# Optimization experiments

Measured on AMD Instinct MI355X. Metric: run time of the kernel, lower is better.

## Reference

```python
import jax, jax.numpy as jnp
import numpy as np

N_SPECIES = 4; N_BASIS = 128; N_GRAPH = 16; R_MAX = 6.0
NS_NODE, NV_NODE = 32, 16          # node irreps 32x0e + 16x1o
NS_EDGE = 16                       # initial edge irreps 16x0e
NS_OUT, NV_OUT = 16, 8             # output irreps 16x0e + 8x1o
NS_IN = 2 * NS_NODE + NS_EDGE      # 80 concatenated scalars
NV_IN = 2 * NV_NODE                # 32 concatenated vectors
NS_CONV = NS_OUT + NV_OUT          # 24 scalars (16 features + 8 gates)
W_SIZES = [NS_IN * NS_CONV, NS_IN * NV_OUT, NV_IN * NV_OUT, NV_IN * NS_CONV, NV_IN * NV_OUT]
N_NODES, N_EDGES = 8192, 65536
EPS = 1e-5


def gaussian_basis(d, stop, n):
    offsets = jnp.linspace(0.0, stop, n)
    coeff = -0.5 / (offsets[1] - offsets[0]) ** 2
    return jnp.exp(coeff * (d[:, None] - offsets[None, :]) ** 2)


def seg_mean(vals, seg, cnt):
    return jax.ops.segment_sum(vals, seg, num_segments=N_GRAPH) / cnt[:, None]


def setup_inputs():
    key = jax.random.key(0)
    ks = jax.random.split(key, 20)
    rn = lambda k, shape, scale: jax.random.normal(k, shape, jnp.float32) * scale
    inp = {}
    inp["node_fea"] = rn(ks[0], (N_NODES, NS_NODE + 3 * NV_NODE), 1.0)
    d = 0.5 + 5.0 * jax.random.uniform(ks[1], (N_EDGES,), jnp.float32)
    vec = jax.random.normal(ks[2], (N_EDGES, 3), jnp.float32)
    inp["edge_attr"] = jnp.concatenate([d[:, None], vec], axis=1)
    inp["edge_index"] = jax.random.randint(ks[3], (2, N_EDGES), 0, N_NODES)
    inp["x"] = jax.random.randint(ks[4], (N_NODES,), 0, N_SPECIES)
    inp["batch"] = jnp.sort(jax.random.randint(ks[5], (N_NODES,), 0, N_GRAPH))
    inp["w_rh"] = rn(ks[6], (N_BASIS, 64), N_BASIS ** -0.5); inp["b_rh"] = jnp.zeros((64,), jnp.float32)
    inp["w_ro"] = rn(ks[7], (64, sum(W_SIZES)), 64 ** -0.5); inp["b_ro"] = jnp.zeros((sum(W_SIZES),), jnp.float32)
    inp["w_pre"] = rn(ks[8], (NS_EDGE, NS_EDGE), NS_EDGE ** -0.5); inp["b_pre"] = jnp.zeros((NS_EDGE,), jnp.float32)
    inp["w_sc"] = rn(ks[9], (NS_EDGE, N_SPECIES ** 2, NS_OUT), 1.0)
    inp["w_post_s"] = rn(ks[10], (NS_OUT, NS_OUT), NS_OUT ** -0.5); inp["b_post_s"] = jnp.zeros((NS_OUT,), jnp.float32)
    inp["w_post_v"] = rn(ks[11], (NV_OUT, NV_OUT), NV_OUT ** -0.5)
    inp["ln_w_s"] = jnp.ones((NS_OUT,), jnp.float32); inp["ln_b_s"] = jnp.zeros((NS_OUT,), jnp.float32)
    inp["ln_w_v"] = jnp.ones((NV_OUT,), jnp.float32)
    inp["w_skip"] = rn(ks[12], (NS_EDGE, NS_OUT), NS_EDGE ** -0.5)
    inp["w_edge_s"] = rn(ks[13], (NS_OUT, NS_OUT), NS_OUT ** -0.5); inp["b_edge_s"] = jnp.zeros((NS_OUT,), jnp.float32)
    inp["w_edge_v"] = rn(ks[14], (NV_OUT, NV_OUT), NV_OUT ** -0.5)
    return inp


def _forward(node_fea, edge_attr, w_rh, b_rh, w_ro, b_ro, w_pre, b_pre, w_sc,
             w_post_s, b_post_s, w_post_v, ln_w_s, ln_b_s, ln_w_v,
             w_skip, w_edge_s, b_edge_s, w_edge_v, edge_index, x, batch):
    E = edge_index.shape[1]
    idx_i, idx_j = edge_index[0], edge_index[1]
    one_hot = jax.nn.one_hot(N_SPECIES * x[idx_i] + x[idx_j], N_SPECIES ** 2, dtype=node_fea.dtype)
    d, vec = edge_attr[:, 0], edge_attr[:, 1:4]
    u = vec / (jnp.linalg.norm(vec, axis=1, keepdims=True) + 1e-12)
    Y1 = np.sqrt(3.0) * u                                   # l=1 sph harm, component norm; Y0 == 1
    rbf = gaussian_basis(d, R_MAX, N_BASIS)                 # edge_length_embedded
    edge_s0 = gaussian_basis(d, 6.0, NS_EDGE)               # distance_expansion -> initial edge scalars
    # self connection: edge scalars x species-pair one-hot -> output scalars
    sc = jnp.einsum('ei,ej,ijo->eo', edge_s0, one_hot, w_sc) / np.sqrt(NS_EDGE * N_SPECIES ** 2)
    edge_s = edge_s0 @ w_pre + b_pre                        # lin_pre
    # gather node features by edge indices and concat
    nf_i, nf_j = node_fea[idx_i], node_fea[idx_j]
    s_in = jnp.concatenate([nf_i[:, :NS_NODE], nf_j[:, :NS_NODE], edge_s], axis=1)  # [E,80]
    v_in = jnp.concatenate([nf_i[:, NS_NODE:].reshape(E, NV_NODE, 3),
                            nf_j[:, NS_NODE:].reshape(E, NV_NODE, 3)], axis=1)      # [E,32,3]
    # radial MLP -> per-edge tensor-product path weights
    h = jax.nn.silu(rbf @ w_rh + b_rh)
    w_all = h @ w_ro + b_ro                                 # [E, 3840]
    w1, w2, w3, w4, w5 = jnp.split(w_all, np.cumsum(W_SIZES)[:-1].tolist(), axis=1)
    # equivariant tensor-product paths (explicit l<=1 Clebsch-Gordan structure)
    s0 = jnp.einsum('ei,eio->eo', s_in, w1.reshape(E, NS_IN, NS_CONV)) / np.sqrt(NS_IN)            # 0e x 0e -> 0e
    vA = jnp.einsum('ei,eio,ec->eoc', s_in, w2.reshape(E, NS_IN, NV_OUT), Y1) / np.sqrt(NS_IN)     # 0e x 1o -> 1o
    vB = jnp.einsum('eic,eio->eoc', v_in, w3.reshape(E, NV_IN, NV_OUT)) / np.sqrt(NV_IN)           # 1o x 0e -> 1o
    s1 = jnp.einsum('eic,eio,ec->eo', v_in, w4.reshape(E, NV_IN, NS_CONV), Y1) / np.sqrt(3.0 * NV_IN)  # 1o.1o -> 0e
    vC = jnp.einsum('eic,eio->eoc', jnp.cross(v_in, Y1[:, None, :]), w5.reshape(E, NV_IN, NV_OUT)) / np.sqrt(2.0 * NV_IN)  # 1o x 1o -> 1o
    s_conv = s0 + s1                                        # [E,24]
    v_conv = vA + vB + vC                                   # [E,8,3]
    # gate nonlinearity inside conv
    s_out = jax.nn.silu(s_conv[:, :NS_OUT])
    v_out = v_conv * jax.nn.sigmoid(s_conv[:, NS_OUT:])[:, :, None]
    # lin_post then self connection
    s_out = s_out @ w_post_s + b_post_s + sc
    v_out = jnp.einsum('eic,io->eoc', v_out, w_post_v)
    # e3LayerNorm keyed by graph id of source node
    eb = batch[idx_i]
    cnt = jnp.maximum(jax.ops.segment_sum(jnp.ones((E,), s_out.dtype), eb, num_segments=N_GRAPH), 1.0)
    mu = seg_mean(s_out, eb, cnt)
    s_c = s_out - mu[eb]
    rms_s = jnp.sqrt(seg_mean(s_c ** 2, eb, cnt).mean(axis=1, keepdims=True) + EPS)
    s_n = s_c / rms_s[eb] * ln_w_s + ln_b_s
    rms_v = jnp.sqrt((seg_mean((v_out ** 2).sum(-1), eb, cnt) / 3.0).mean(axis=1, keepdims=True) + EPS)
    v_n = v_out / rms_v[eb][:, :, None] * ln_w_v[None, :, None]
    # skip connection from old edge features (scalars only)
    s_n = s_n + edge_s0 @ w_skip
    # final lin_edge
    s_fin = s_n @ w_edge_s + b_edge_s
    v_fin = jnp.einsum('eic,io->eoc', v_n, w_edge_v)
    return jnp.concatenate([s_fin, v_fin.reshape(E, NV_OUT * 3)], axis=1)  # [E,40]


def reference(node_fea, edge_attr, edge_index, x, batch, w_rh, b_rh, w_ro, b_ro,
              w_pre, b_pre, w_sc, w_post_s, b_post_s, w_post_v, ln_w_s, ln_b_s, ln_w_v,
              w_skip, w_edge_s, b_edge_s, w_edge_v):
    return _forward(node_fea, edge_attr, w_rh, b_rh, w_ro, b_ro, w_pre, b_pre, w_sc,
                    w_post_s, b_post_s, w_post_v, ln_w_s, ln_b_s, ln_w_v,
                    w_skip, w_edge_s, b_edge_s, w_edge_v, edge_index, x, batch)
```

## Files before the change

kernel.cpp:

```cpp
#include <hip/hip_runtime.h>

typedef unsigned short u16;
typedef unsigned int u32;
typedef __attribute__((ext_vector_type(8))) _Float16 half8;
typedef __attribute__((ext_vector_type(2))) __fp16 fp16x2;
typedef __attribute__((ext_vector_type(4))) float floatx4;

#define E_TOTAL 65536

__device__ __forceinline__ u32 pk16(float x0, float x1) {
    union { fp16x2 h; u32 u; } c;
    c.h = __builtin_amdgcn_cvt_pkrtz(x0, x1);
    return c.u;
}
union Frag8h { u32 u[4]; half8 v; };


__global__ void k_zero(float* __restrict__ ws) {
    const int i = threadIdx.x + blockIdx.x * blockDim.x;
    if (i < 1056) ws[i] = 0.0f;
}

__global__ __launch_bounds__(64) void k_probe(int* __restrict__ binv) {
    const int lane = threadIdx.x;
    const int q = lane >> 4;
    if (lane < 32) binv[lane] = lane;
    half8 bfr;
    #pragma unroll
    for (int j = 0; j < 8; ++j) bfr[j] = (_Float16)(float)(q*8 + j + 1);
    #pragma unroll
    for (int s = 0; s < 32; ++s) {
        const int qa = s >> 3, ja = s & 7;
        half8 afr;
        #pragma unroll
        for (int j = 0; j < 8; ++j) afr[j] = (_Float16)0.0f;
        if (q == qa) afr[ja] = (_Float16)1.0f;
        floatx4 dc = {0.0f, 0.0f, 0.0f, 0.0f};
        dc = __builtin_amdgcn_mfma_f32_16x16x32_f16(afr, bfr, dc, 0, 0, 0);
        if (lane == 0) {
            const int sB = (int)(dc[0] + 0.5f) - 1;
            if (sB >= 0 && sB < 32) binv[sB] = s;
        }
    }
}

__global__ __launch_bounds__(256) void k_edge_heavy(
    const float* __restrict__ node_fea, const float* __restrict__ edge_attr,
    const int* __restrict__ edge_index, const int* __restrict__ xsp,
    const float* __restrict__ w_rh, const float* __restrict__ b_rh,
    const float* __restrict__ w_ro, const float* __restrict__ b_ro,
    const float* __restrict__ w_pre, const float* __restrict__ b_pre,
    const float* __restrict__ w_sc, const float* __restrict__ w_post_s,
    const float* __restrict__ b_post_s, const float* __restrict__ w_post_v,
    const int* __restrict__ binv,
    float* __restrict__ out)
{
    __shared__ __align__(16) u16 a_rbf[16 * 128];
    __shared__ __align__(16) u16 a_h[16 * 64];
    __shared__ __align__(16) float sh_wt[16][258];
    __shared__ float sh_sin[16][80];
    __shared__ float sh_vl[16][3][32];
    __shared__ float sh_acc[16][56];
    __shared__ float sh_es0[16][16];
    __shared__ float sh_y1[16][4];
    __shared__ int   sh_kmap[32];

    const int tid = threadIdx.x;
    const int ed = tid >> 4, l16 = tid & 15;
    const int lane = tid & 63, w = tid >> 6;
    const int quad = lane >> 4, l15 = lane & 15;
    const int e = blockIdx.x * 16 + ed;

    if (tid < 32) sh_kmap[tid] = binv[tid];

    const int ni = edge_index[e];
    const int nj = edge_index[E_TOTAL + e];
    const float4 ea = *(const float4*)(edge_attr + 4*e);
    const float d  = ea.x;
    const float vx = ea.y, vy = ea.z, vz = ea.w;
    const float invn = 1.0f / (sqrtf(vx*vx + vy*vy + vz*vz) + 1e-12f);
    const float Y0 = 1.7320508075688772f * vx * invn;
    const float Y1 = 1.7320508075688772f * vy * invn;
    const float Y2 = 1.7320508075688772f * vz * invn;
    if (l16 == 0) { sh_y1[ed][0] = Y0; sh_y1[ed][1] = Y1; sh_y1[ed][2] = Y2; }

    const float C128 = -0.5f * (127.0f/6.0f) * (127.0f/6.0f);
    const float S128 = 6.0f/127.0f;
    {
        Frag8h thi;
        #pragma unroll
        for (int r2 = 0; r2 < 4; ++r2) {
            const int b0i = l16*8 + 2*r2;
            const float t0 = d - S128 * (float)b0i;
            const float t1 = d - S128 * (float)(b0i + 1);
            const float x0 = expf(C128 * t0 * t0);
            const float x1 = expf(C128 * t1 * t1);
            thi.u[r2] = pk16(x0, x1);
        }
        *(half8*)&a_rbf[(l16*16 + ed)*8] = thi.v;
    }
    {
        const float t = d - 0.4f * (float)l16;
        sh_es0[ed][l16] = expf(-3.125f * t * t);
    }

    const float rs80 = 0.11180339887498949f;
    const float rs32 = 0.17677669529663689f;
    {
        const float* fi = node_fea + (size_t)ni * 80;
        const float* fj = node_fea + (size_t)nj * 80;
        sh_sin[ed][2*l16+0]    = fi[2*l16+0] * rs80;
        sh_sin[ed][2*l16+1]    = fi[2*l16+1] * rs80;
        sh_sin[ed][32+2*l16+0] = fj[2*l16+0] * rs80;
        sh_sin[ed][32+2*l16+1] = fj[2*l16+1] * rs80;
        #pragma unroll
        for (int c = 0; c < 3; ++c) {
            sh_vl[ed][c][l16]      = fi[32 + 3*l16 + c] * rs32;
            sh_vl[ed][c][16 + l16] = fj[32 + 3*l16 + c] * rs32;
        }
    }
    for (int s = tid; s < 16*56; s += 256) (&sh_acc[0][0])[s] = 0.0f;
    __syncthreads();

    int km[8];
    u32 voff0[8], voff1[8];
    #pragma unroll
    for (int j = 0; j < 8; ++j) {
        km[j] = sh_kmap[quad*8 + j];
        voff0[j] = (u32)(km[j] * 3840 + l15);
        voff1[j] = voff0[j] + 32u * 3840u;
    }

    float my_sc;
    {
        const int o = l16;
        float es = b_pre[o];
        float sc = 0.0f;
        const int p = 4*xsp[ni] + xsp[nj];
        #pragma unroll
        for (int i = 0; i < 16; ++i) {
            const float g = sh_es0[ed][i];
            es += g * w_pre[i*16 + o];
            sc += g * w_sc[(i*16 + p)*16 + o];
        }
        sh_sin[ed][64 + o] = es * rs80;
        my_sc = sc * 0.0625f;
    }

    {
        floatx4 hacc = {0.0f, 0.0f, 0.0f, 0.0f};
        #pragma unroll
        for (int kk = 0; kk < 4; ++kk) {
            const half8 ah = *(const half8*)&a_rbf[((kk*4 + quad)*16 + l15)*8];
            Frag8h bh;
            #pragma unroll
            for (int jj = 0; jj < 4; ++jj) {
                const float x0 = w_rh[(size_t)(kk*32 + km[2*jj+0])*64 + w*16 + l15];
                const float x1 = w_rh[(size_t)(kk*32 + km[2*jj+1])*64 + w*16 + l15];
                bh.u[jj] = pk16(x0, x1);
            }
            hacc = __builtin_amdgcn_mfma_f32_16x16x32_f16(ah, bh.v, hacc, 0, 0, 0);
        }
        const int hn = w*16 + l15;
        const float bb = b_rh[hn];
        const int k8 = hn >> 3, j2 = hn & 7;
        #pragma unroll
        for (int r = 0; r < 4; ++r) {
            const float x = hacc[r] + bb;
            const float s = x / (1.0f + expf(-x));
            const int m = quad*4 + r;
            union { _Float16 h; u16 u; } cv; cv.h = (_Float16)s;
            a_h[(k8*16 + m)*8 + j2] = cv.u;
        }
    }
    __syncthreads();

    const half8 a0 = *(const half8*)&a_h[((0*4 + quad)*16 + l15)*8];
    const half8 a1 = *(const half8*)&a_h[((1*4 + quad)*16 + l15)*8];

    for (int ch = 0; ch < 15; ++ch) {
        const int coff = ch * 256;
        floatx4 acc[4];
        float bias[4];
        #pragma unroll
        for (int ct = 0; ct < 4; ++ct) {
            const int sgct = __builtin_amdgcn_readfirstlane(ch*16 + w*4 + ct);
            const float* bp = w_ro + sgct*16;
            float f0[8], f1[8];
            #pragma unroll
            for (int j = 0; j < 8; ++j) {
                f0[j] = bp[voff0[j]];
                f1[j] = bp[voff1[j]];
            }
            Frag8h b0, b1;
            #pragma unroll
            for (int jj = 0; jj < 4; ++jj) {
                b0.u[jj] = pk16(f0[2*jj], f0[2*jj+1]);
                b1.u[jj] = pk16(f1[2*jj], f1[2*jj+1]);
            }
            floatx4 a = {0.0f, 0.0f, 0.0f, 0.0f};
            a = __builtin_amdgcn_mfma_f32_16x16x32_f16(a0, b0.v, a, 0, 0, 0);
            a = __builtin_amdgcn_mfma_f32_16x16x32_f16(a1, b1.v, a, 0, 0, 0);
            acc[ct] = a;
            bias[ct] = b_ro[sgct*16 + l15];
        }
        __syncthreads();
        #pragma unroll
        for (int ct = 0; ct < 4; ++ct) {
            const int col = w*64 + ct*16 + l15;
            #pragma unroll
            for (int r = 0; r < 4; ++r)
                sh_wt[quad*4 + r][col] = acc[ct][r] + bias[ct];
        }
        __syncthreads();

        if (ch <= 7) {
            const int hi = (ch == 7) ? 1920 : (coff + 256);
            for (int idx = tid; idx < 384; idx += 256) {
                const int eo = idx / 24, o = idx % 24;
                const int i0 = (coff > o) ? (coff - o + 23) / 24 : 0;
                int i1 = (hi - o + 23) / 24; if (i1 > 80) i1 = 80;
                float a = 0.0f;
                for (int i = i0; i < i1; ++i)
                    a += sh_sin[eo][i] * sh_wt[eo][i*24 + o - coff];
                sh_acc[eo][o] += a;
            }
        }
        if (ch == 7) {
            for (int idx = tid; idx < 128; idx += 256) {
                const int eo = idx >> 3, o = idx & 7;
                float a = 0.0f;
                #pragma unroll
                for (int i = 0; i < 16; ++i)
                    a += sh_sin[eo][i] * sh_wt[eo][128 + i*8 + o];
                sh_acc[eo][24 + o] += a;
            }
        }
        if (ch == 8 || ch == 9) {
            const int ib = (ch == 8) ? 16 : 48;
            for (int idx = tid; idx < 128; idx += 256) {
                const int eo = idx >> 3, o = idx & 7;
                float a = 0.0f;
                #pragma unroll
                for (int i2 = 0; i2 < 32; ++i2)
                    a += sh_sin[eo][ib + i2] * sh_wt[eo][i2*8 + o];
                sh_acc[eo][24 + o] += a;
            }
        }
        if (ch == 10) {
            for (int idx = tid; idx < 384; idx += 256) {
                const int eo = idx / 24, rem = idx % 24;
                const int o = rem / 3, cc = rem % 3;
                float a = 0.0f;
                #pragma unroll
                for (int i = 0; i < 32; ++i)
                    a += sh_vl[eo][cc][i] * sh_wt[eo][i*8 + o];
                sh_acc[eo][32 + o*3 + cc] += a;
            }
        }
        if (ch >= 11 && ch <= 13) {
            const int rel = coff - 2816;
            for (int idx = tid; idx < 384; idx += 256) {
                const int eo = idx / 24, o = idx % 24;
                const int i0 = (rel > o) ? (rel - o + 23) / 24 : 0;
                int i1 = (rel + 256 - o + 23) / 24; if (i1 > 32) i1 = 32;
                const float Ya = sh_y1[eo][0], Yb = sh_y1[eo][1], Yc = sh_y1[eo][2];
                float a = 0.0f;
                for (int i = i0; i < i1; ++i) {
                    const float qv = sh_vl[eo][0][i]*Ya + sh_vl[eo][1][i]*Yb
                                   + sh_vl[eo][2][i]*Yc;
                    a += qv * sh_wt[eo][i*24 + o - rel];
                }
                sh_acc[eo][o] += a * 0.57735026918962573f;
            }
        }
        if (ch == 14) {
            for (int idx = tid; idx < 384; idx += 256) {
                const int eo = idx / 24, rem = idx % 24;
                const int o = rem / 3, cc = rem % 3;
                const int c1 = (cc < 2) ? cc + 1 : 0;
                const int c2 = (c1 < 2) ? c1 + 1 : 0;
                const float Yp = sh_y1[eo][c2];
                const float Ym = sh_y1[eo][c1];
                float a = 0.0f;
                #pragma unroll
                for (int i = 0; i < 32; ++i)
                    a += (sh_vl[eo][c1][i]*Yp - sh_vl[eo][c2][i]*Ym) * sh_wt[eo][i*8 + o];
                sh_acc[eo][32 + o*3 + cc] += a * 0.70710678118654746f;
            }
        }
    }
    __syncthreads();

    {
        const int o = l16;
        float a = b_post_s[o] + my_sc;
        #pragma unroll
        for (int i = 0; i < 16; ++i) {
            const float sv = sh_acc[ed][i];
            a += (sv / (1.0f + expf(-sv))) * w_post_s[i*16 + o];
        }
        out[(size_t)e*40 + o] = a;
    }
    if (l16 < 8) {
        const int o = l16;
        const float Ya = sh_y1[ed][0], Yb = sh_y1[ed][1], Yc = sh_y1[ed][2];
        float r0 = 0.0f, r1 = 0.0f, r2 = 0.0f;
        #pragma unroll
        for (int i = 0; i < 8; ++i) {
            const float g  = 1.0f / (1.0f + expf(-sh_acc[ed][16 + i]));
            const float a2 = sh_acc[ed][24 + i];
            const float ww = w_post_v[i*8 + o];
            r0 += (a2*Ya + sh_acc[ed][32 + i*3 + 0]) * g * ww;
            r1 += (a2*Yb + sh_acc[ed][32 + i*3 + 1]) * g * ww;
            r2 += (a2*Yc + sh_acc[ed][32 + i*3 + 2]) * g * ww;
        }
        out[(size_t)e*40 + 16 + o*3 + 0] = r0;
        out[(size_t)e*40 + 16 + o*3 + 1] = r1;
        out[(size_t)e*40 + 16 + o*3 + 2] = r2;
    }
}

__global__ __launch_bounds__(256) void k_stats_partial(
    const float* __restrict__ sv, const int* __restrict__ edge_index,
    const int* __restrict__ batch, float* __restrict__ ws)
{
    __shared__ float bins[768];
    const int tid = threadIdx.x;
    for (int s = tid; s < 768; s += 256) bins[s] = 0.0f;
    __syncthreads();

    const int e = blockIdx.x * 256 + tid;
    const int g = batch[edge_index[e]];
    const float* p = sv + (size_t)e * 40;
    float v[40];
    #pragma unroll
    for (int j = 0; j < 40; ++j) v[j] = p[j];

    float* bg = bins + g * 48;
    #pragma unroll
    for (int chn = 0; chn < 16; ++chn) {
        atomicAdd(&bg[chn],      v[chn]);
        atomicAdd(&bg[16 + chn], v[chn] * v[chn]);
    }
    #pragma unroll
    for (int o = 0; o < 8; ++o) {
        const float a = v[16 + o*3], b = v[16 + o*3 + 1], c = v[16 + o*3 + 2];
        atomicAdd(&bg[32 + o], a*a + b*b + c*c);
    }
    atomicAdd(&bg[40], 1.0f);
    __syncthreads();

    for (int s = tid; s < 768; s += 256) {
        const float x = bins[s];
        if (x != 0.0f) atomicAdd(&ws[s], x);
    }
}

__global__ __launch_bounds__(64) void k_stats_final(float* __restrict__ ws)
{
    const int tid = threadIdx.x;
    if (tid < 16) {
        const int g = tid;
        float cnt = ws[g*48 + 40]; if (cnt < 1.0f) cnt = 1.0f;
        const float ic = 1.0f / cnt;
        float vs = 0.0f;
        for (int chn = 0; chn < 16; ++chn) {
            const float mu = ws[g*48 + chn] * ic;
            ws[768 + g*16 + chn] = mu;
            vs += ws[g*48 + 16 + chn] * ic - mu * mu;
        }
        if (vs < 0.0f) vs = 0.0f;
        ws[1024 + g] = 1.0f / sqrtf(vs * (1.0f/16.0f) + 1e-5f);
        float vv = 0.0f;
        for (int o = 0; o < 8; ++o) vv += ws[g*48 + 32 + o];
        vv = vv * ic * (1.0f/3.0f) * (1.0f/8.0f);
        ws[1040 + g] = 1.0f / sqrtf(vv + 1e-5f);
    }
}

__global__ __launch_bounds__(256) void k_edge_final(
    float* buf, const float* __restrict__ ws,
    const float* __restrict__ edge_attr, const int* __restrict__ edge_index,
    const int* __restrict__ batch,
    const float* __restrict__ ln_w_s, const float* __restrict__ ln_b_s,
    const float* __restrict__ ln_w_v, const float* __restrict__ w_skip,
    const float* __restrict__ w_edge_s, const float* __restrict__ b_edge_s,
    const float* __restrict__ w_edge_v)
{
    __shared__ float sh_mu[16][16];
    __shared__ float sh_is[16], sh_iv[16];
    __shared__ float sh_lws[16], sh_lbs[16], sh_lwv[8];
    __shared__ float sh_skip[16][16], sh_wes[16][16], sh_bes[16], sh_wev[8][8];
    const int tid = threadIdx.x;
    sh_mu[tid >> 4][tid & 15]   = ws[768 + tid];
    sh_skip[tid >> 4][tid & 15] = w_skip[tid];
    sh_wes[tid >> 4][tid & 15]  = w_edge_s[tid];
    if (tid < 16) {
        sh_is[tid]  = ws[1024 + tid];
        sh_iv[tid]  = ws[1040 + tid];
        sh_lws[tid] = ln_w_s[tid];
        sh_lbs[tid] = ln_b_s[tid];
        sh_bes[tid] = b_edge_s[tid];
    }
    if (tid < 8)  sh_lwv[tid] = ln_w_v[tid];
    if (tid < 64) sh_wev[tid >> 3][tid & 7] = w_edge_v[tid];
    __syncthreads();

    const int e = blockIdx.x * 256 + tid;
    const int g = batch[edge_index[e]];
    const float d = edge_attr[4*e];
    float es0[16];
    #pragma unroll
    for (int b = 0; b < 16; ++b) {
        const float t = d - 0.4f * (float)b;
        es0[b] = expf(-3.125f * t * t);
    }
    float p[40];
    float* pb = buf + (size_t)e * 40;
    #pragma unroll
    for (int j = 0; j < 40; ++j) p[j] = pb[j];

    const float is = sh_is[g];
    float sn[16];
    #pragma unroll
    for (int chn = 0; chn < 16; ++chn)
        sn[chn] = (p[chn] - sh_mu[g][chn]) * is * sh_lws[chn] + sh_lbs[chn];
    #pragma unroll
    for (int b = 0; b < 16; ++b) {
        const float g0 = es0[b];
        #pragma unroll
        for (int chn = 0; chn < 16; ++chn) sn[chn] += g0 * sh_skip[b][chn];
    }
    #pragma unroll
    for (int o = 0; o < 16; ++o) {
        float a = sh_bes[o];
        #pragma unroll
        for (int chn = 0; chn < 16; ++chn) a += sn[chn] * sh_wes[chn][o];
        pb[o] = a;
    }
    const float iv = sh_iv[g];
    float vn[8][3];
    #pragma unroll
    for (int i = 0; i < 8; ++i) {
        const float f = iv * sh_lwv[i];
        vn[i][0] = p[16 + i*3 + 0] * f;
        vn[i][1] = p[16 + i*3 + 1] * f;
        vn[i][2] = p[16 + i*3 + 2] * f;
    }
    #pragma unroll
    for (int o = 0; o < 8; ++o) {
        float r0 = 0.0f, r1 = 0.0f, r2 = 0.0f;
        #pragma unroll
        for (int i = 0; i < 8; ++i) {
            const float w = sh_wev[i][o];
            r0 += vn[i][0] * w; r1 += vn[i][1] * w; r2 += vn[i][2] * w;
        }
        pb[16 + o*3 + 0] = r0;
        pb[16 + o*3 + 1] = r1;
        pb[16 + o*3 + 2] = r2;
    }
}

extern "C" void kernel_launch(void* const* d_in, const int* in_sizes, int n_in,
                              void* d_out, int out_size, void* d_ws, size_t ws_size,
                              hipStream_t stream)
{
    const float* node_fea  = (const float*)d_in[0];
    const float* edge_attr = (const float*)d_in[1];
    const int* edge_index  = (const int*)d_in[2];
    const int* xsp         = (const int*)d_in[3];
    const int* batch       = (const int*)d_in[4];
    const float* w_rh      = (const float*)d_in[5];
    const float* b_rh      = (const float*)d_in[6];
    const float* w_ro      = (const float*)d_in[7];
    const float* b_ro      = (const float*)d_in[8];
    const float* w_pre     = (const float*)d_in[9];
    const float* b_pre     = (const float*)d_in[10];
    const float* w_sc      = (const float*)d_in[11];
    const float* w_post_s  = (const float*)d_in[12];
    const float* b_post_s  = (const float*)d_in[13];
    const float* w_post_v  = (const float*)d_in[14];
    const float* ln_w_s    = (const float*)d_in[15];
    const float* ln_b_s    = (const float*)d_in[16];
    const float* ln_w_v    = (const float*)d_in[17];
    const float* w_skip    = (const float*)d_in[18];
    const float* w_edge_s  = (const float*)d_in[19];
    const float* b_edge_s  = (const float*)d_in[20];
    const float* w_edge_v  = (const float*)d_in[21];

    float* ws   = (float*)d_ws;
    int*   binv = (int*)(ws + 1056);
    float* out  = (float*)d_out;

    k_zero<<<2, 1024, 0, stream>>>(ws);
    k_probe<<<1, 64, 0, stream>>>(binv);
    k_edge_heavy<<<4096, 256, 0, stream>>>(node_fea, edge_attr, edge_index, xsp,
        w_rh, b_rh, w_ro, b_ro, w_pre, b_pre, w_sc, w_post_s, b_post_s, w_post_v,
        binv, out);
    k_stats_partial<<<256, 256, 0, stream>>>(out, edge_index, batch, ws);
    k_stats_final<<<1, 64, 0, stream>>>(ws);
    k_edge_final<<<256, 256, 0, stream>>>(out, ws, edge_attr, edge_index,
        batch, ln_w_s, ln_b_s, ln_w_v, w_skip, w_edge_s, b_edge_s, w_edge_v);
}
```

Measured before the change: 460.0 us.

## Process 32 edges per block to reuse w_ro fragments; merge small kernels

The heavy edge kernel now handles two 16-edge groups per block. Each w_ro B-fragment loaded from global memory feeds MFMAs for both groups, which halves the weight-fetch traffic per edge, and the grid shrinks to 2048 blocks. The zero and probe kernels are merged into one, and the stats-final computation is folded into the prologue of the final edge kernel, which removes two launches. In exchange, shared memory per block roughly doubles (sh_wt is now 32x258 floats) and register pressure rises, which can lower occupancy.

```diff
diff --git a/kernel.cpp b/kernel.cpp
--- a/kernel.cpp
+++ b/kernel.cpp
@@ -16,30 +16,29 @@
 union Frag8h { u32 u[4]; half8 v; };
 
 
-__global__ void k_zero(float* __restrict__ ws) {
-    const int i = threadIdx.x + blockIdx.x * blockDim.x;
-    if (i < 1056) ws[i] = 0.0f;
-}
-
-__global__ __launch_bounds__(64) void k_probe(int* __restrict__ binv) {
-    const int lane = threadIdx.x;
-    const int q = lane >> 4;
-    if (lane < 32) binv[lane] = lane;
-    half8 bfr;
-    #pragma unroll
-    for (int j = 0; j < 8; ++j) bfr[j] = (_Float16)(float)(q*8 + j + 1);
-    #pragma unroll
-    for (int s = 0; s < 32; ++s) {
-        const int qa = s >> 3, ja = s & 7;
-        half8 afr;
-        #pragma unroll
-        for (int j = 0; j < 8; ++j) afr[j] = (_Float16)0.0f;
-        if (q == qa) afr[ja] = (_Float16)1.0f;
-        floatx4 dc = {0.0f, 0.0f, 0.0f, 0.0f};
-        dc = __builtin_amdgcn_mfma_f32_16x16x32_f16(afr, bfr, dc, 0, 0, 0);
-        if (lane == 0) {
-            const int sB = (int)(dc[0] + 0.5f) - 1;
-            if (sB >= 0 && sB < 32) binv[sB] = s;
+__global__ __launch_bounds__(1024) void k_init(float* __restrict__ ws, int* __restrict__ binv) {
+    const int tid = threadIdx.x;
+    for (int i = tid; i < 1056; i += 1024) ws[i] = 0.0f;
+    if (tid < 64) {
+        const int lane = tid;
+        const int q = lane >> 4;
+        if (lane < 32) binv[lane] = lane;
+        half8 bfr;
+        #pragma unroll
+        for (int j = 0; j < 8; ++j) bfr[j] = (_Float16)(float)(q*8 + j + 1);
+        #pragma unroll
+        for (int s = 0; s < 32; ++s) {
+            const int qa = s >> 3, ja = s & 7;
+            half8 afr;
+            #pragma unroll
+            for (int j = 0; j < 8; ++j) afr[j] = (_Float16)0.0f;
+            if (q == qa) afr[ja] = (_Float16)1.0f;
+            floatx4 dc = {0.0f, 0.0f, 0.0f, 0.0f};
+            dc = __builtin_amdgcn_mfma_f32_16x16x32_f16(afr, bfr, dc, 0, 0, 0);
+            if (lane == 0) {
+                const int sB = (int)(dc[0] + 0.5f) - 1;
+                if (sB >= 0 && sB < 32) binv[sB] = s;
+            }
         }
     }
 }
@@ -55,60 +54,72 @@
     const int* __restrict__ binv,
     float* __restrict__ out)
 {
-    __shared__ __align__(16) u16 a_rbf[16 * 128];
-    __shared__ __align__(16) u16 a_h[16 * 64];
-    __shared__ __align__(16) float sh_wt[16][258];
-    __shared__ float sh_sin[16][80];
-    __shared__ float sh_vl[16][3][32];
-    __shared__ float sh_acc[16][56];
-    __shared__ float sh_es0[16][16];
-    __shared__ float sh_y1[16][4];
+    __shared__ __align__(16) u16 a_rbf[2 * 2048];
+    __shared__ __align__(16) u16 a_h[2 * 1024];
+    __shared__ __align__(16) float sh_wt[32][258];
+    __shared__ float sh_sin[32][80];
+    __shared__ float sh_vl[32][3][32];
+    __shared__ float sh_acc[32][56];
+    __shared__ float sh_es0[32][16];
+    __shared__ float sh_y1[32][4];
     __shared__ int   sh_kmap[32];
 
     const int tid = threadIdx.x;
     const int ed = tid >> 4, l16 = tid & 15;
     const int lane = tid & 63, w = tid >> 6;
     const int quad = lane >> 4, l15 = lane & 15;
-    const int e = blockIdx.x * 16 + ed;
+    const int e0 = blockIdx.x * 32 + ed;
+    const int e1 = e0 + 16;
 
     if (tid < 32) sh_kmap[tid] = binv[tid];
 
-    const int ni = edge_index[e];
-    const int nj = edge_index[E_TOTAL + e];
-    const float4 ea = *(const float4*)(edge_attr + 4*e);
-    const float d  = ea.x;
-    const float vx = ea.y, vy = ea.z, vz = ea.w;
-    const float invn = 1.0f / (sqrtf(vx*vx + vy*vy + vz*vz) + 1e-12f);
-    const float Y0 = 1.7320508075688772f * vx * invn;
-    const float Y1 = 1.7320508075688772f * vy * invn;
-    const float Y2 = 1.7320508075688772f * vz * invn;
-    if (l16 == 0) { sh_y1[ed][0] = Y0; sh_y1[ed][1] = Y1; sh_y1[ed][2] = Y2; }
+    const int ni0 = edge_index[e0], nj0 = edge_index[E_TOTAL + e0];
+    const int ni1 = edge_index[e1], nj1 = edge_index[E_TOTAL + e1];
+    const float4 ea0 = *(const float4*)(edge_attr + 4*e0);
+    const float4 ea1 = *(const float4*)(edge_attr + 4*e1);
+    const float d0 = ea0.x, d1 = ea1.x;
+    {
+        const float invn0 = 1.0f / (sqrtf(ea0.y*ea0.y + ea0.z*ea0.z + ea0.w*ea0.w) + 1e-12f);
+        const float invn1 = 1.0f / (sqrtf(ea1.y*ea1.y + ea1.z*ea1.z + ea1.w*ea1.w) + 1e-12f);
+        if (l16 == 0) {
+            sh_y1[ed][0]    = 1.7320508075688772f * ea0.y * invn0;
+            sh_y1[ed][1]    = 1.7320508075688772f * ea0.z * invn0;
+            sh_y1[ed][2]    = 1.7320508075688772f * ea0.w * invn0;
+            sh_y1[16+ed][0] = 1.7320508075688772f * ea1.y * invn1;
+            sh_y1[16+ed][1] = 1.7320508075688772f * ea1.z * invn1;
+            sh_y1[16+ed][2] = 1.7320508075688772f * ea1.w * invn1;
+        }
+    }
 
     const float C128 = -0.5f * (127.0f/6.0f) * (127.0f/6.0f);
     const float S128 = 6.0f/127.0f;
     {
-        Frag8h thi;
+        Frag8h t0, t1;
         #pragma unroll
         for (int r2 = 0; r2 < 4; ++r2) {
             const int b0i = l16*8 + 2*r2;
-            const float t0 = d - S128 * (float)b0i;
-            const float t1 = d - S128 * (float)(b0i + 1);
-            const float x0 = expf(C128 * t0 * t0);
-            const float x1 = expf(C128 * t1 * t1);
-            thi.u[r2] = pk16(x0, x1);
-        }
-        *(half8*)&a_rbf[(l16*16 + ed)*8] = thi.v;
-    }
-    {
-        const float t = d - 0.4f * (float)l16;
-        sh_es0[ed][l16] = expf(-3.125f * t * t);
+            const float u0 = d0 - S128 * (float)b0i;
+            const float u1 = d0 - S128 * (float)(b0i + 1);
+            const float v0 = d1 - S128 * (float)b0i;
+            const float v1 = d1 - S128 * (float)(b0i + 1);
+            t0.u[r2] = pk16(expf(C128*u0*u0), expf(C128*u1*u1));
+            t1.u[r2] = pk16(expf(C128*v0*v0), expf(C128*v1*v1));
+        }
+        *(half8*)&a_rbf[(l16*16 + ed)*8]        = t0.v;
+        *(half8*)&a_rbf[2048 + (l16*16 + ed)*8] = t1.v;
+    }
+    {
+        const float t0 = d0 - 0.4f * (float)l16;
+        const float t1 = d1 - 0.4f * (float)l16;
+        sh_es0[ed][l16]    = expf(-3.125f * t0 * t0);
+        sh_es0[16+ed][l16] = expf(-3.125f * t1 * t1);
     }
 
     const float rs80 = 0.11180339887498949f;
     const float rs32 = 0.17677669529663689f;
     {
-        const float* fi = node_fea + (size_t)ni * 80;
-        const float* fj = node_fea + (size_t)nj * 80;
+        const float* fi = node_fea + (size_t)ni0 * 80;
+        const float* fj = node_fea + (size_t)nj0 * 80;
         sh_sin[ed][2*l16+0]    = fi[2*l16+0] * rs80;
         sh_sin[ed][2*l16+1]    = fi[2*l16+1] * rs80;
         sh_sin[ed][32+2*l16+0] = fj[2*l16+0] * rs80;
@@ -119,7 +130,20 @@
             sh_vl[ed][c][16 + l16] = fj[32 + 3*l16 + c] * rs32;
         }
     }
-    for (int s = tid; s < 16*56; s += 256) (&sh_acc[0][0])[s] = 0.0f;
+    {
+        const float* fi = node_fea + (size_t)ni1 * 80;
+        const float* fj = node_fea + (size_t)nj1 * 80;
+        sh_sin[16+ed][2*l16+0]    = fi[2*l16+0] * rs80;
+        sh_sin[16+ed][2*l16+1]    = fi[2*l16+1] * rs80;
+        sh_sin[16+ed][32+2*l16+0] = fj[2*l16+0] * rs80;
+        sh_sin[16+ed][32+2*l16+1] = fj[2*l16+1] * rs80;
+        #pragma unroll
+        for (int c = 0; c < 3; ++c) {
+            sh_vl[16+ed][c][l16]      = fi[32 + 3*l16 + c] * rs32;
+            sh_vl[16+ed][c][16 + l16] = fj[32 + 3*l16 + c] * rs32;
+        }
+    }
+    for (int s = tid; s < 32*56; s += 256) (&sh_acc[0][0])[s] = 0.0f;
     __syncthreads();
 
     int km[8];
@@ -131,27 +155,35 @@
         voff1[j] = voff0[j] + 32u * 3840u;
     }
 
-    float my_sc;
+    float my_sc0, my_sc1;
     {
         const int o = l16;
-        float es = b_pre[o];
-        float sc = 0.0f;
-        const int p = 4*xsp[ni] + xsp[nj];
+        float es0v = b_pre[o], sc0 = 0.0f;
+        float es1v = b_pre[o], sc1 = 0.0f;
+        const int p0 = 4*xsp[ni0] + xsp[nj0];
+        const int p1 = 4*xsp[ni1] + xsp[nj1];
         #pragma unroll
         for (int i = 0; i < 16; ++i) {
-            const float g = sh_es0[ed][i];
-            es += g * w_pre[i*16 + o];
-            sc += g * w_sc[(i*16 + p)*16 + o];
-        }
-        sh_sin[ed][64 + o] = es * rs80;
-        my_sc = sc * 0.0625f;
-    }
-
-    {
-        floatx4 hacc = {0.0f, 0.0f, 0.0f, 0.0f};
+            const float g0 = sh_es0[ed][i];
+            const float g1 = sh_es0[16+ed][i];
+            es0v += g0 * w_pre[i*16 + o];
+            es1v += g1 * w_pre[i*16 + o];
+            sc0  += g0 * w_sc[(i*16 + p0)*16 + o];
+            sc1  += g1 * w_sc[(i*16 + p1)*16 + o];
+        }
+        sh_sin[ed][64 + o]    = es0v * rs80;
+        sh_sin[16+ed][64 + o] = es1v * rs80;
+        my_sc0 = sc0 * 0.0625f;
+        my_sc1 = sc1 * 0.0625f;
+    }
+
+    {
+        floatx4 h0 = {0.0f, 0.0f, 0.0f, 0.0f};
+        floatx4 h1 = {0.0f, 0.0f, 0.0f, 0.0f};
         #pragma unroll
         for (int kk = 0; kk < 4; ++kk) {
-            const half8 ah = *(const half8*)&a_rbf[((kk*4 + quad)*16 + l15)*8];
+            const half8 ag0 = *(const half8*)&a_rbf[((kk*4 + quad)*16 + l15)*8];
+            const half8 ag1 = *(const half8*)&a_rbf[2048 + ((kk*4 + quad)*16 + l15)*8];
             Frag8h bh;
             #pragma unroll
             for (int jj = 0; jj < 4; ++jj) {
@@ -159,28 +191,39 @@
                 const float x1 = w_rh[(size_t)(kk*32 + km[2*jj+1])*64 + w*16 + l15];
                 bh.u[jj] = pk16(x0, x1);
             }
-            hacc = __builtin_amdgcn_mfma_f32_16x16x32_f16(ah, bh.v, hacc, 0, 0, 0);
+            h0 = __builtin_amdgcn_mfma_f32_16x16x32_f16(ag0, bh.v, h0, 0, 0, 0);
+            h1 = __builtin_amdgcn_mfma_f32_16x16x32_f16(ag1, bh.v, h1, 0, 0, 0);
         }
         const int hn = w*16 + l15;
         const float bb = b_rh[hn];
         const int k8 = hn >> 3, j2 = hn & 7;
         #pragma unroll
         for (int r = 0; r < 4; ++r) {
-            const float x = hacc[r] + bb;
-            const float s = x / (1.0f + expf(-x));
             const int m = quad*4 + r;
-            union { _Float16 h; u16 u; } cv; cv.h = (_Float16)s;
-            a_h[(k8*16 + m)*8 + j2] = cv.u;
+            {
+                const float x = h0[r] + bb;
+                const float s = x / (1.0f + expf(-x));
+                union { _Float16 h; u16 u; } cv; cv.h = (_Float16)s;
+                a_h[(k8*16 + m)*8 + j2] = cv.u;
+            }
+            {
+                const float x = h1[r] + bb;
+                const float s = x / (1.0f + expf(-x));
+                union { _Float16 h; u16 u; } cv; cv.h = (_Float16)s;
+                a_h[1024 + (k8*16 + m)*8 + j2] = cv.u;
+            }
         }
     }
     __syncthreads();
 
-    const half8 a0 = *(const half8*)&a_h[((0*4 + quad)*16 + l15)*8];
-    const half8 a1 = *(const half8*)&a_h[((1*4 + quad)*16 + l15)*8];
+    const half8 a0g0 = *(const half8*)&a_h[((0*4 + quad)*16 + l15)*8];
+    const half8 a1g0 = *(const half8*)&a_h[((1*4 + quad)*16 + l15)*8];
+    const half8 a0g1 = *(const half8*)&a_h[1024 + ((0*4 + quad)*16 + l15)*8];
+    const half8 a1g1 = *(const half8*)&a_h[1024 + ((1*4 + quad)*16 + l15)*8];
 
     for (int ch = 0; ch < 15; ++ch) {
         const int coff = ch * 256;
-        floatx4 acc[4];
+        floatx4 acc0[4], acc1[4];
         float bias[4];
         #pragma unroll
         for (int ct = 0; ct < 4; ++ct) {
@@ -199,9 +242,13 @@
                 b1.u[jj] = pk16(f1[2*jj], f1[2*jj+1]);
             }
             floatx4 a = {0.0f, 0.0f, 0.0f, 0.0f};
-            a = __builtin_amdgcn_mfma_f32_16x16x32_f16(a0, b0.v, a, 0, 0, 0);
-            a = __builtin_amdgcn_mfma_f32_16x16x32_f16(a1, b1.v, a, 0, 0, 0);
-            acc[ct] = a;
+            a = __builtin_amdgcn_mfma_f32_16x16x32_f16(a0g0, b0.v, a, 0, 0, 0);
+            a = __builtin_amdgcn_mfma_f32_16x16x32_f16(a1g0, b1.v, a, 0, 0, 0);
+            acc0[ct] = a;
+            floatx4 c = {0.0f, 0.0f, 0.0f, 0.0f};
+            c = __builtin_amdgcn_mfma_f32_16x16x32_f16(a0g1, b0.v, c, 0, 0, 0);
+            c = __builtin_amdgcn_mfma_f32_16x16x32_f16(a1g1, b1.v, c, 0, 0, 0);
+            acc1[ct] = c;
             bias[ct] = b_ro[sgct*16 + l15];
         }
         __syncthreads();
@@ -209,14 +256,16 @@
         for (int ct = 0; ct < 4; ++ct) {
             const int col = w*64 + ct*16 + l15;
             #pragma unroll
-            for (int r = 0; r < 4; ++r)
-                sh_wt[quad*4 + r][col] = acc[ct][r] + bias[ct];
+            for (int r = 0; r < 4; ++r) {
+                sh_wt[quad*4 + r][col]      = acc0[ct][r] + bias[ct];
+                sh_wt[16 + quad*4 + r][col] = acc1[ct][r] + bias[ct];
+            }
         }
         __syncthreads();
 
         if (ch <= 7) {
             const int hi = (ch == 7) ? 1920 : (coff + 256);
-            for (int idx = tid; idx < 384; idx += 256) {
+            for (int idx = tid; idx < 768; idx += 256) {
                 const int eo = idx / 24, o = idx % 24;
                 const int i0 = (coff > o) ? (coff - o + 23) / 24 : 0;
                 int i1 = (hi - o + 23) / 24; if (i1 > 80) i1 = 80;
@@ -227,7 +276,7 @@
             }
         }
         if (ch == 7) {
-            for (int idx = tid; idx < 128; idx += 256) {
+            for (int idx = tid; idx < 256; idx += 256) {
                 const int eo = idx >> 3, o = idx & 7;
                 float a = 0.0f;
                 #pragma unroll
@@ -238,7 +287,7 @@
         }
         if (ch == 8 || ch == 9) {
             const int ib = (ch == 8) ? 16 : 48;
-            for (int idx = tid; idx < 128; idx += 256) {
+            for (int idx = tid; idx < 256; idx += 256) {
                 const int eo = idx >> 3, o = idx & 7;
                 float a = 0.0f;
                 #pragma unroll
@@ -248,7 +297,7 @@
             }
         }
         if (ch == 10) {
-            for (int idx = tid; idx < 384; idx += 256) {
+            for (int idx = tid; idx < 768; idx += 256) {
                 const int eo = idx / 24, rem = idx % 24;
                 const int o = rem / 3, cc = rem % 3;
                 float a = 0.0f;
@@ -260,7 +309,7 @@
         }
         if (ch >= 11 && ch <= 13) {
             const int rel = coff - 2816;
-            for (int idx = tid; idx < 384; idx += 256) {
+            for (int idx = tid; idx < 768; idx += 256) {
                 const int eo = idx / 24, o = idx % 24;
                 const int i0 = (rel > o) ? (rel - o + 23) / 24 : 0;
                 int i1 = (rel + 256 - o + 23) / 24; if (i1 > 32) i1 = 32;
@@ -275,7 +324,7 @@
             }
         }
         if (ch == 14) {
-            for (int idx = tid; idx < 384; idx += 256) {
+            for (int idx = tid; idx < 768; idx += 256) {
                 const int eo = idx / 24, rem = idx % 24;
                 const int o = rem / 3, cc = rem % 3;
                 const int c1 = (cc < 2) ? cc + 1 : 0;
@@ -292,32 +341,38 @@
     }
     __syncthreads();
 
-    {
-        const int o = l16;
-        float a = b_post_s[o] + my_sc;
-        #pragma unroll
-        for (int i = 0; i < 16; ++i) {
-            const float sv = sh_acc[ed][i];
-            a += (sv / (1.0f + expf(-sv))) * w_post_s[i*16 + o];
-        }
-        out[(size_t)e*40 + o] = a;
-    }
-    if (l16 < 8) {
-        const int o = l16;
-        const float Ya = sh_y1[ed][0], Yb = sh_y1[ed][1], Yc = sh_y1[ed][2];
-        float r0 = 0.0f, r1 = 0.0f, r2 = 0.0f;
-        #pragma unroll
-        for (int i = 0; i < 8; ++i) {
-            const float g  = 1.0f / (1.0f + expf(-sh_acc[ed][16 + i]));
-            const float a2 = sh_acc[ed][24 + i];
-            const float ww = w_post_v[i*8 + o];
-            r0 += (a2*Ya + sh_acc[ed][32 + i*3 + 0]) * g * ww;
-            r1 += (a2*Yb + sh_acc[ed][32 + i*3 + 1]) * g * ww;
-            r2 += (a2*Yc + sh_acc[ed][32 + i*3 + 2]) * g * ww;
-        }
-        out[(size_t)e*40 + 16 + o*3 + 0] = r0;
-        out[(size_t)e*40 + 16 + o*3 + 1] = r1;
-        out[(size_t)e*40 + 16 + o*3 + 2] = r2;
+    #pragma unroll
+    for (int g = 0; g < 2; ++g) {
+        const int er = g*16 + ed;
+        const int e  = (g == 0) ? e0 : e1;
+        const float msc = (g == 0) ? my_sc0 : my_sc1;
+        {
+            const int o = l16;
+            float a = b_post_s[o] + msc;
+            #pragma unroll
+            for (int i = 0; i < 16; ++i) {
+                const float sv = sh_acc[er][i];
+                a += (sv / (1.0f + expf(-sv))) * w_post_s[i*16 + o];
+            }
+            out[(size_t)e*40 + o] = a;
+        }
+        if (l16 < 8) {
+            const int o = l16;
+            const float Ya = sh_y1[er][0], Yb = sh_y1[er][1], Yc = sh_y1[er][2];
+            float r0 = 0.0f, r1 = 0.0f, r2 = 0.0f;
+            #pragma unroll
+            for (int i = 0; i < 8; ++i) {
+                const float gt = 1.0f / (1.0f + expf(-sh_acc[er][16 + i]));
+                const float a2 = sh_acc[er][24 + i];
+                const float ww = w_post_v[i*8 + o];
+                r0 += (a2*Ya + sh_acc[er][32 + i*3 + 0]) * gt * ww;
+                r1 += (a2*Yb + sh_acc[er][32 + i*3 + 1]) * gt * ww;
+                r2 += (a2*Yc + sh_acc[er][32 + i*3 + 2]) * gt * ww;
+            }
+            out[(size_t)e*40 + 16 + o*3 + 0] = r0;
+            out[(size_t)e*40 + 16 + o*3 + 1] = r1;
+            out[(size_t)e*40 + 16 + o*3 + 2] = r2;
+        }
     }
 }
 
@@ -354,28 +409,6 @@
     for (int s = tid; s < 768; s += 256) {
         const float x = bins[s];
         if (x != 0.0f) atomicAdd(&ws[s], x);
-    }
-}
-
-__global__ __launch_bounds__(64) void k_stats_final(float* __restrict__ ws)
-{
-    const int tid = threadIdx.x;
-    if (tid < 16) {
-        const int g = tid;
-        float cnt = ws[g*48 + 40]; if (cnt < 1.0f) cnt = 1.0f;
-        const float ic = 1.0f / cnt;
-        float vs = 0.0f;
-        for (int chn = 0; chn < 16; ++chn) {
-            const float mu = ws[g*48 + chn] * ic;
-            ws[768 + g*16 + chn] = mu;
-            vs += ws[g*48 + 16 + chn] * ic - mu * mu;
-        }
-        if (vs < 0.0f) vs = 0.0f;
-        ws[1024 + g] = 1.0f / sqrtf(vs * (1.0f/16.0f) + 1e-5f);
-        float vv = 0.0f;
-        for (int o = 0; o < 8; ++o) vv += ws[g*48 + 32 + o];
-        vv = vv * ic * (1.0f/3.0f) * (1.0f/8.0f);
-        ws[1040 + g] = 1.0f / sqrtf(vv + 1e-5f);
     }
 }
 
@@ -393,12 +426,26 @@
     __shared__ float sh_lws[16], sh_lbs[16], sh_lwv[8];
     __shared__ float sh_skip[16][16], sh_wes[16][16], sh_bes[16], sh_wev[8][8];
     const int tid = threadIdx.x;
-    sh_mu[tid >> 4][tid & 15]   = ws[768 + tid];
+    if (tid < 16) {
+        const int g = tid;
+        float cnt = ws[g*48 + 40]; if (cnt < 1.0f) cnt = 1.0f;
+        const float ic = 1.0f / cnt;
+        float vs = 0.0f;
+        for (int chn = 0; chn < 16; ++chn) {
+            const float mu = ws[g*48 + chn] * ic;
+            sh_mu[g][chn] = mu;
+            vs += ws[g*48 + 16 + chn] * ic - mu * mu;
+        }
+        if (vs < 0.0f) vs = 0.0f;
+        sh_is[g] = 1.0f / sqrtf(vs * (1.0f/16.0f) + 1e-5f);
+        float vv = 0.0f;
+        for (int o = 0; o < 8; ++o) vv += ws[g*48 + 32 + o];
+        vv = vv * ic * (1.0f/3.0f) * (1.0f/8.0f);
+        sh_iv[g] = 1.0f / sqrtf(vv + 1e-5f);
+    }
     sh_skip[tid >> 4][tid & 15] = w_skip[tid];
     sh_wes[tid >> 4][tid & 15]  = w_edge_s[tid];
     if (tid < 16) {
-        sh_is[tid]  = ws[1024 + tid];
-        sh_iv[tid]  = ws[1040 + tid];
         sh_lws[tid] = ln_w_s[tid];
         sh_lbs[tid] = ln_b_s[tid];
         sh_bes[tid] = b_edge_s[tid];
@@ -493,13 +540,11 @@
     int*   binv = (int*)(ws + 1056);
     float* out  = (float*)d_out;
 
-    k_zero<<<2, 1024, 0, stream>>>(ws);
-    k_probe<<<1, 64, 0, stream>>>(binv);
-    k_edge_heavy<<<4096, 256, 0, stream>>>(node_fea, edge_attr, edge_index, xsp,
+    k_init<<<1, 1024, 0, stream>>>(ws, binv);
+    k_edge_heavy<<<2048, 256, 0, stream>>>(node_fea, edge_attr, edge_index, xsp,
         w_rh, b_rh, w_ro, b_ro, w_pre, b_pre, w_sc, w_post_s, b_post_s, w_post_v,
         binv, out);
     k_stats_partial<<<256, 256, 0, stream>>>(out, edge_index, batch, ws);
-    k_stats_final<<<1, 64, 0, stream>>>(ws);
     k_edge_final<<<256, 256, 0, stream>>>(out, ws, edge_attr, edge_index,
         batch, ln_w_s, ln_b_s, ln_w_v, w_skip, w_edge_s, b_edge_s, w_edge_v);
 }
```

Result: slower. 558.5 us (+21.4%).
